# Performance work log

Hardware: AMD Instinct MI355X
Metric: run time of the kernel (lower is better)

## Reference

```python
import jax, jax.numpy as jnp
import numpy as np

B, TQ, TKV, D, H = 4, 1024, 2048, 1024, 16
DH = D // H


def setup_inputs() -> dict:
    key = jax.random.key(0)
    ks = jax.random.split(key, 12)
    s = 0.02
    return {
        "x": jax.random.normal(ks[0], (B, TQ, D), jnp.float32),
        "k_cache": jax.random.normal(ks[1], (B, TKV, D), jnp.float32),
        "v_cache": jax.random.normal(ks[2], (B, TKV, D), jnp.float32),
        "mask": jnp.zeros((TQ, TKV), jnp.float32),  # additive attention bias
        "Wq": jax.random.normal(ks[3], (D, D), jnp.float32) * s,
        "bq": jax.random.normal(ks[4], (D,), jnp.float32) * s,
        "Wk": jax.random.normal(ks[5], (D, D), jnp.float32) * s,  # key: no bias (Whisper-style)
        "Wv": jax.random.normal(ks[6], (D, D), jnp.float32) * s,
        "bv": jax.random.normal(ks[7], (D,), jnp.float32) * s,
        "Wo": jax.random.normal(ks[8], (D, D), jnp.float32) * s,
        "bo": jax.random.normal(ks[9], (D,), jnp.float32) * s,
    }


def reference(x, k_cache, v_cache, mask, Wq, bq, Wk, Wv, bv, Wo, bo):
    b, tq, d = x.shape
    scale = (d // H) ** -0.25
    # QKV projections (torch Linear: y = x @ W.T + b)
    q = x @ Wq.T + bq                      # [B,Tq,D]
    k_new = x @ Wk.T                       # [B,Tq,D] (key has no bias)
    v_new = x @ Wv.T + bv                  # [B,Tq,D]
    # KV-cache append: write last Tq positions
    k_cache = k_cache.at[:, -tq:, :].set(k_new)
    v_cache = v_cache.at[:, -tq:, :].set(v_new)
    # split heads
    qh = q.reshape(b, tq, H, DH) * scale           # [B,Tq,H,Dh]
    kh = k_cache.reshape(b, -1, H, DH) * scale     # [B,Tkv,H,Dh]
    vh = v_cache.reshape(b, -1, H, DH)             # [B,Tkv,H,Dh]
    qk = jnp.einsum("bqhd,bkhd->bhqk", qh, kh) + mask  # [B,H,Tq,Tkv]
    w = jax.nn.softmax(qk.astype(jnp.float32), axis=-1).astype(qh.dtype)
    wv = jnp.einsum("bhqk,bkhd->bqhd", w, vh).reshape(b, tq, d)
    out = wv @ Wo.T + bo
    return out, k_cache, v_cache
```

## Files before the change

kernel.cpp:

```cpp
#include <hip/hip_runtime.h>
#include <hip/hip_bf16.h>


typedef __bf16 bf16_t;
typedef __attribute__((ext_vector_type(4))) float f32x4;
typedef __attribute__((ext_vector_type(8))) __bf16 bf16x8;
typedef __attribute__((ext_vector_type(4))) __bf16 bf16x4;
typedef __attribute__((ext_vector_type(4))) unsigned short u16x4;

__device__ inline bf16x4 cvt4(float4 f) {
    bf16x4 o;
    o.x = (bf16_t)f.x; o.y = (bf16_t)f.y; o.z = (bf16_t)f.z; o.w = (bf16_t)f.w;
    return o;
}

__device__ inline void gload_lds16(const void* g, void* s) {
    __builtin_amdgcn_global_load_lds(
        (const __attribute__((address_space(1))) void*)g,
        (__attribute__((address_space(3))) void*)s, 16, 0, 0);
}

__device__ inline unsigned cvt_pk_bf16(float lo, float hi) {
    unsigned r;
    asm("v_cvt_pk_bf16_f32 %0, %1, %2" : "=v"(r) : "v"(lo), "v"(hi));
    return r;
}
__device__ inline void pswap32(unsigned& a, unsigned& b) {
    asm("v_permlane32_swap_b32 %0, %1" : "+v"(a), "+v"(b));
}
__device__ inline void pswap16(unsigned& a, unsigned& b) {
    asm("v_permlane16_swap_b32 %0, %1" : "+v"(a), "+v"(b));
}

#if __has_builtin(__builtin_amdgcn_exp2f)
__device__ inline float exp2_fast(float x) { return __builtin_amdgcn_exp2f(x); }
#else
__device__ inline float exp2_fast(float x) { return exp2f(x); }
#endif


__global__ void cast_f32_bf16_k(const float* __restrict__ src, bf16_t* __restrict__ dst, int n4) {
    int i = blockIdx.x * blockDim.x + threadIdx.x;
    if (i >= n4) return;
    float4 f = reinterpret_cast<const float4*>(src)[i];
    reinterpret_cast<bf16x4*>(dst)[i] = cvt4(f);
}

__global__ void build_wqkv_k(const float* __restrict__ Wq, const float* __restrict__ Wk,
                             const float* __restrict__ Wv, bf16_t* __restrict__ dst) {
    int i = blockIdx.x * blockDim.x + threadIdx.x;
    if (i >= 786432) return;
    int e0 = i * 4;
    int row = e0 >> 10;
    const float* src;
    if (row < 1024)       src = Wq + e0;
    else if (row < 2048)  src = Wk + (e0 - 1048576);
    else                  src = Wv + (e0 - 2097152);
    float4 f = *reinterpret_cast<const float4*>(src);
    reinterpret_cast<bf16x4*>(dst)[i] = cvt4(f);
}

__global__ void build_bias_k(const float* __restrict__ bq, const float* __restrict__ bv,
                             float* __restrict__ bias) {
    int i = blockIdx.x * blockDim.x + threadIdx.x;
    if (i >= 3072) return;
    float v;
    if (i < 1024)      v = bq[i];
    else if (i < 2048) v = 0.f;
    else               v = bv[i - 2048];
    bias[i] = v;
}

__global__ void copy_old2_k(const float* __restrict__ kc, const float* __restrict__ vc,
                            float* __restrict__ kout, float* __restrict__ vout,
                            bf16_t* __restrict__ k_bf) {
    int i = blockIdx.x * blockDim.x + threadIdx.x;
    if (i >= 2097152) return;
    int which = i >> 20;
    int ii = i & 1048575;
    int b = ii >> 18;
    int r = ii & 262143;
    size_t off = (size_t)b * 2097152 + (size_t)r * 4;
    if (which == 0) {
        float4 f = *reinterpret_cast<const float4*>(kc + off);
        *reinterpret_cast<float4*>(kout + off) = f;
        reinterpret_cast<bf16x4*>(k_bf + off)[0] = cvt4(f);
    } else {
        float4 f = *reinterpret_cast<const float4*>(vc + off);
        *reinterpret_cast<float4*>(vout + off) = f;
    }
}

__global__ __launch_bounds__(256) void transpose_v_k(const float* __restrict__ vout,
                                                     bf16_t* __restrict__ vT) {
    __shared__ bf16_t t[64][65];
    int blk = blockIdx.x;
    int kvt = blk >> 6;
    int bh  = blk & 63;
    int b = bh >> 4, h = bh & 15;
    int kv0 = kvt * 64;
    int tid = threadIdx.x;
    int c = tid & 63, r0 = tid >> 6;
    #pragma unroll
    for (int rr = r0; rr < 64; rr += 4)
        t[rr][c] = (bf16_t)vout[((size_t)b * 2048 + kv0 + rr) * 1024 + h * 64 + c];
    __syncthreads();
    #pragma unroll
    for (int dd = r0; dd < 64; dd += 4)
        vT[((size_t)bh * 64 + dd) * 2048 + kv0 + c] = t[c][dd];
}

__global__ void mask_bf16_k(const float* __restrict__ mask, bf16_t* __restrict__ maskB) {
    int i = blockIdx.x * blockDim.x + threadIdx.x;
    if (i >= 2097152) return;
    int r   = i & 3;
    int c16 = (i >> 2) & 15;
    int qd  = (i >> 6) & 3;
    int kb  = (i >> 8) & 127;
    int qb  = i >> 15;
    float v = mask[(size_t)(qb * 16 + c16) * 2048 + kb * 16 + qd * 4 + r] * 1.4426950408889634f;
    maskB[i] = (bf16_t)v;
}

template <int MODE>
__global__ __launch_bounds__(256) void gemm_lds_k(const bf16_t* __restrict__ A,
                                                  const bf16_t* __restrict__ Bw,
                                                  const float* __restrict__ bias,
                                                  bf16_t* __restrict__ q_bf,
                                                  float* __restrict__ kout,
                                                  bf16_t* __restrict__ k_bf,
                                                  float* __restrict__ vout,
                                                  float* __restrict__ out0) {
    const int K = 1024;
    __shared__ __align__(16) bf16_t As[2][4096];
    __shared__ __align__(16) bf16_t Bs[2][4096];
    int m0 = blockIdx.x * 128, n0 = blockIdx.y * 128;
    int tid = threadIdx.x;
    int lane = tid & 63, w = tid >> 6;
    int wr = w >> 1, wc = w & 1;
    int col16 = lane & 15, quad = lane >> 4;
    int mbase = m0 + wr * 64, nbase = n0 + wc * 64;

    int srow = tid >> 2;
    int scol = (tid & 3) * 8;
    const bf16_t* ga = A + (size_t)(m0 + srow) * K + scol;
    const bf16_t* gb = Bw + (size_t)(n0 + srow) * K + scol;

    f32x4 zero = {0.f, 0.f, 0.f, 0.f};
    f32x4 acc[4][4];
    #pragma unroll
    for (int mi = 0; mi < 4; mi++)
        #pragma unroll
        for (int ni = 0; ni < 4; ni++) acc[mi][ni] = zero;

    auto stageg = [&](int d, int k) {
        gload_lds16(ga + k, &As[d][tid * 8]);
        gload_lds16(ga + (size_t)64 * K + k, &As[d][tid * 8 + 2048]);
        gload_lds16(gb + k, &Bs[d][tid * 8]);
        gload_lds16(gb + (size_t)64 * K + k, &Bs[d][tid * 8 + 2048]);
    };

    stageg(0, 0);
    __syncthreads();
    for (int kb = 0; kb < 32; kb++) {
        int cur = kb & 1;
        if (kb < 31) stageg(cur ^ 1, (kb + 1) * 32);
        bf16x8 af[4], bfr[4];
        #pragma unroll
        for (int mi = 0; mi < 4; mi++)
            af[mi] = *reinterpret_cast<const bf16x8*>(
                &As[cur][(wr * 64 + mi * 16 + col16) * 32 + quad * 8]);
        #pragma unroll
        for (int ni = 0; ni < 4; ni++)
            bfr[ni] = *reinterpret_cast<const bf16x8*>(
                &Bs[cur][(wc * 64 + ni * 16 + col16) * 32 + quad * 8]);
        #pragma unroll
        for (int mi = 0; mi < 4; mi++)
            #pragma unroll
            for (int ni = 0; ni < 4; ni++)
                acc[mi][ni] = __builtin_amdgcn_mfma_f32_16x16x32_bf16(
                    af[mi], bfr[ni], acc[mi][ni], 0, 0, 0);
        __syncthreads();
    }

    #pragma unroll
    for (int mi = 0; mi < 4; mi++) {
        #pragma unroll
        for (int ni = 0; ni < 4; ni++) {
            int gm_base = mbase + mi * 16 + quad * 4;
            int gn = nbase + ni * 16 + col16;
            float bia = bias[gn];
            #pragma unroll
            for (int r = 0; r < 4; r++) {
                int gm = gm_base + r;
                float v = acc[mi][ni][r] + bia;
                if (MODE == 0) {
                    if (gn < 1024) {
                        q_bf[(size_t)gm * 1024 + gn] = (bf16_t)v;
                    } else if (gn < 2048) {
                        int n2 = gn - 1024;
                        int b = gm >> 10, t = gm & 1023;
                        size_t off = ((size_t)b * 2048 + 1024 + t) * 1024 + n2;
                        kout[off] = v;
                        k_bf[off] = (bf16_t)v;
                    } else {
                        int n2 = gn - 2048;
                        int b = gm >> 10, t = gm & 1023;
                        vout[((size_t)b * 2048 + 1024 + t) * 1024 + n2] = v;
                    }
                } else {
                    out0[(size_t)gm * 1024 + gn] = v;
                }
            }
        }
    }
}

__global__ __launch_bounds__(512, 4) void attn_k(const bf16_t* __restrict__ qbf,
                                                 const bf16_t* __restrict__ kbf,
                                                 const bf16_t* __restrict__ vT,
                                                 const bf16_t* __restrict__ maskB,
                                                 bf16_t* __restrict__ wv) {
    __shared__ __align__(16) bf16_t Ks[2][4096];
    __shared__ __align__(16) bf16_t Vs[2][4096];
    int logical = (blockIdx.x & 7) * 64 + (blockIdx.x >> 3);
    int bh = logical >> 3;
    int qtb = logical & 7;
    int b = bh >> 4, h = bh & 15;
    int tid = threadIdx.x, w = tid >> 6, lane = tid & 63;
    int col16 = lane & 15, quad = lane >> 4;
    int c7 = col16 & 7;
    int cx = (quad ^ c7) * 8;
    int qr0 = qtb * 128 + w * 16;

    int sr = tid >> 3, sc = (tid & 7) ^ ((tid >> 3) & 7);
    const bf16_t* kg = kbf + ((size_t)b * 2048 + sr) * 1024 + h * 64 + sc * 8;
    const bf16_t* vg = vT + ((size_t)bh * 64 + sr) * 2048 + sc * 8;
    auto stage = [&](int d, int kv0) {
        gload_lds16(kg + (size_t)kv0 * 1024, &Ks[d][tid * 8]);
        gload_lds16(vg + kv0, &Vs[d][tid * 8]);
    };

    const bf16_t* qrow = qbf + ((size_t)b * 1024 + qr0 + col16) * 1024 + h * 64;
    bf16x8 aq0 = *reinterpret_cast<const bf16x8*>(qrow + quad * 8);
    bf16x8 aq1 = *reinterpret_cast<const bf16x8*>(qrow + 32 + quad * 8);

    const bf16_t* mbase = maskB + (size_t)(qtb * 8 + w) * 32768 + quad * 64 + col16 * 4;

    f32x4 zero = {0.f, 0.f, 0.f, 0.f};
    f32x4 oacc[4];
    #pragma unroll
    for (int dt = 0; dt < 4; dt++) oacc[dt] = zero;
    float lrow = 0.f;

    stage(0, 0);
    __syncthreads();

    for (int t = 0; t < 32; t++) {
        int cur = t & 1;
        if (t < 31) stage(cur ^ 1, (t + 1) * 64);
        unsigned pk[4][2];
        #pragma unroll
        for (int nt = 0; nt < 4; nt++) {
            const bf16_t* kr = &Ks[cur][(nt * 16 + col16) * 64];
            bf16x8 k0 = *reinterpret_cast<const bf16x8*>(kr + cx);
            bf16x8 k1 = *reinterpret_cast<const bf16x8*>(kr + (cx ^ 32));
            f32x4 s = __builtin_amdgcn_mfma_f32_16x16x32_bf16(k0, aq0, zero, 0, 0, 0);
            s = __builtin_amdgcn_mfma_f32_16x16x32_bf16(k1, aq1, s, 0, 0, 0);
            u16x4 m4 = *reinterpret_cast<const u16x4*>(mbase + (size_t)(t * 4 + nt) * 256);
            float p[4];
            #pragma unroll
            for (int r = 0; r < 4; r++) {
                float mv = __builtin_bit_cast(float, (unsigned)m4[r] << 16);
                p[r] = exp2_fast(fmaf(s[r], 0.18033688011112042f, mv));
                lrow += p[r];
            }
            pk[nt][0] = cvt_pk_bf16(p[0], p[1]);
            pk[nt][1] = cvt_pk_bf16(p[2], p[3]);
        }
        union PB { unsigned u[4]; bf16x8 v; };
        PB pf0, pf1;
        {
            unsigned a0 = pk[0][0], b0 = pk[1][0];
            pswap32(a0, b0); pswap16(a0, b0);
            pf0.u[0] = a0; pf0.u[2] = b0;
            unsigned a1 = pk[0][1], b1 = pk[1][1];
            pswap32(a1, b1); pswap16(a1, b1);
            pf0.u[1] = a1; pf0.u[3] = b1;
            unsigned a2 = pk[2][0], b2 = pk[3][0];
            pswap32(a2, b2); pswap16(a2, b2);
            pf1.u[0] = a2; pf1.u[2] = b2;
            unsigned a3 = pk[2][1], b3 = pk[3][1];
            pswap32(a3, b3); pswap16(a3, b3);
            pf1.u[1] = a3; pf1.u[3] = b3;
        }
        #pragma unroll
        for (int dt = 0; dt < 4; dt++) {
            const bf16_t* vr = &Vs[cur][(dt * 16 + col16) * 64];
            bf16x8 v0 = *reinterpret_cast<const bf16x8*>(vr + cx);
            bf16x8 v1 = *reinterpret_cast<const bf16x8*>(vr + (cx ^ 32));
            oacc[dt] = __builtin_amdgcn_mfma_f32_16x16x32_bf16(v0, pf0.v, oacc[dt], 0, 0, 0);
            oacc[dt] = __builtin_amdgcn_mfma_f32_16x16x32_bf16(v1, pf1.v, oacc[dt], 0, 0, 0);
        }
        __syncthreads();
    }

    lrow += __shfl_xor(lrow, 16);
    lrow += __shfl_xor(lrow, 32);
    float inv = 1.f / lrow;
    bf16_t* orow = wv + ((size_t)b * 1024 + qr0 + col16) * 1024 + h * 64 + quad * 4;
    #pragma unroll
    for (int dt = 0; dt < 4; dt++) {
        bf16x4 o4;
        #pragma unroll
        for (int r = 0; r < 4; r++) o4[r] = (bf16_t)(oacc[dt][r] * inv);
        *reinterpret_cast<bf16x4*>(orow + dt * 16) = o4;
    }
}


extern "C" void kernel_launch(void* const* d_in, const int* in_sizes, int n_in,
                              void* d_out, int out_size, void* d_ws, size_t ws_size,
                              hipStream_t stream) {
    const float* x    = (const float*)d_in[0];
    const float* kc   = (const float*)d_in[1];
    const float* vc   = (const float*)d_in[2];
    const float* mask = (const float*)d_in[3];
    const float* Wq   = (const float*)d_in[4];
    const float* bq   = (const float*)d_in[5];
    const float* Wk   = (const float*)d_in[6];
    const float* Wv   = (const float*)d_in[7];
    const float* bv   = (const float*)d_in[8];
    const float* Wo   = (const float*)d_in[9];
    const float* bo   = (const float*)d_in[10];

    float* out0 = (float*)d_out;
    float* kout = out0 + 4194304;
    float* vout = out0 + 12582912;

    char* ws = (char*)d_ws;
    bf16_t* x_bf     = (bf16_t*)(ws);
    bf16_t* wqkv_bf  = (bf16_t*)(ws + 8388608);
    bf16_t* wo_bf    = (bf16_t*)(ws + 14680064);
    float*  bias_qkv = (float*)(ws + 16777216);
    bf16_t* q_bf     = (bf16_t*)(ws + 16789504);
    bf16_t* k_bf     = (bf16_t*)(ws + 25178112);
    bf16_t* vT_bf    = (bf16_t*)(ws + 41955328);
    bf16_t* wv_bf    = (bf16_t*)(ws + 58732544);
    bf16_t* maskB    = (bf16_t*)(ws + 67108864);

    cast_f32_bf16_k<<<4096, 256, 0, stream>>>(x, x_bf, 1048576);
    build_wqkv_k<<<3072, 256, 0, stream>>>(Wq, Wk, Wv, wqkv_bf);
    cast_f32_bf16_k<<<1024, 256, 0, stream>>>(Wo, wo_bf, 262144);
    build_bias_k<<<12, 256, 0, stream>>>(bq, bv, bias_qkv);
    mask_bf16_k<<<8192, 256, 0, stream>>>(mask, maskB);
    copy_old2_k<<<8192, 256, 0, stream>>>(kc, vc, kout, vout, k_bf);
    gemm_lds_k<0><<<dim3(32, 24), 256, 0, stream>>>(x_bf, wqkv_bf, bias_qkv,
                                                    q_bf, kout, k_bf, vout, nullptr);
    transpose_v_k<<<2048, 256, 0, stream>>>(vout, vT_bf);
    attn_k<<<512, 512, 0, stream>>>(q_bf, k_bf, vT_bf, maskB, wv_bf);
    gemm_lds_k<1><<<dim3(32, 8), 256, 0, stream>>>(wv_bf, wo_bf, bo,
                                                   nullptr, nullptr, nullptr, nullptr, out0);
}
```

Before: 313.5 us.

## Use 256x256-tile 8-wave pipelined GEMM for QKV projection; swizzle LDS in Wo GEMM

Replaces the QKV projection GEMM with a 256x256-tile, 512-thread kernel using BK=64. It uses XOR-swizzled LDS layouts, staggered A/B prefetch with explicit vmcnt waits, and barrier-separated MFMA phases with s_setprio. The Wo GEMM keeps its 128x128 tiling but gains an XOR swizzle on LDS reads and writes to reduce bank conflicts, and both epilogues are reordered so bias is loaded once per column. The aim is more data reuse per tile and better overlap of loads with MFMA. The cost is only 192 blocks for the QKV GEMM, which lowers occupancy, plus 128 KB of LDS per block.

Result: no change. 316.2 us (+0.9%).

```diff
diff --git a/kernel.cpp b/kernel.cpp
--- a/kernel.cpp
+++ b/kernel.cpp
@@ -122,15 +122,201 @@
     maskB[i] = (bf16_t)v;
 }
 
-template <int MODE>
-__global__ __launch_bounds__(256) void gemm_lds_k(const bf16_t* __restrict__ A,
+#define LDF(bufp, row, off) (*reinterpret_cast<const bf16x8*>(&(bufp)[(row) * 64 + (off)]))
+
+__global__ __launch_bounds__(512, 2) void gemm8_k(const bf16_t* __restrict__ A,
                                                   const bf16_t* __restrict__ Bw,
                                                   const float* __restrict__ bias,
                                                   bf16_t* __restrict__ q_bf,
                                                   float* __restrict__ kout,
                                                   bf16_t* __restrict__ k_bf,
-                                                  float* __restrict__ vout,
-                                                  float* __restrict__ out0) {
+                                                  float* __restrict__ vout) {
+    const int K = 1024;
+    __shared__ __align__(16) bf16_t As[2][16384];
+    __shared__ __align__(16) bf16_t Bs[2][16384];
+    int m0 = blockIdx.x * 256, n0 = blockIdx.y * 256;
+    int tid = threadIdx.x;
+    int lane = tid & 63, w = tid >> 6;
+    int wrM = w >> 2, wrN = w & 3;
+    int col16 = lane & 15, quad = lane >> 4;
+    int cx = (quad ^ (col16 & 7)) * 8;
+
+    int sr = tid >> 3;
+    int scb = ((tid & 7) ^ (sr & 7)) * 8;
+    const bf16_t* ga = A + (size_t)(m0 + sr) * K + scb;
+    const bf16_t* gb = Bw + (size_t)(n0 + sr) * K + scb;
+    int ldst = sr * 64 + (tid & 7) * 8;
+
+    auto stageA = [&](int d, int kt) {
+        size_t ko = (size_t)kt * 64;
+        gload_lds16(ga + ko, &As[d][ldst]);
+        gload_lds16(ga + 64 * (size_t)K + ko, &As[d][ldst + 4096]);
+        gload_lds16(ga + 128 * (size_t)K + ko, &As[d][ldst + 8192]);
+        gload_lds16(ga + 192 * (size_t)K + ko, &As[d][ldst + 12288]);
+    };
+    auto stageB = [&](int d, int kt) {
+        size_t ko = (size_t)kt * 64;
+        gload_lds16(gb + ko, &Bs[d][ldst]);
+        gload_lds16(gb + 64 * (size_t)K + ko, &Bs[d][ldst + 4096]);
+        gload_lds16(gb + 128 * (size_t)K + ko, &Bs[d][ldst + 8192]);
+        gload_lds16(gb + 192 * (size_t)K + ko, &Bs[d][ldst + 12288]);
+    };
+
+    int arow = wrM * 128 + col16;
+    int brow = wrN * 64 + col16;
+
+    f32x4 zero = {0.f, 0.f, 0.f, 0.f};
+    f32x4 acc[8][4];
+    #pragma unroll
+    for (int mi = 0; mi < 8; mi++)
+        #pragma unroll
+        for (int ni = 0; ni < 4; ni++) acc[mi][ni] = zero;
+
+    stageA(0, 0);
+    stageB(0, 0);
+    stageA(1, 1);
+    asm volatile("s_waitcnt vmcnt(4)" ::: "memory");
+    __builtin_amdgcn_s_barrier();
+
+    for (int kt = 0; kt < 16; kt++) {
+        int d = kt & 1;
+        const bf16_t* Ad = As[d];
+        const bf16_t* Bd = Bs[d];
+        bf16x8 a0[4][2], bb0[2][2];
+        #pragma unroll
+        for (int mi = 0; mi < 4; mi++) {
+            a0[mi][0] = LDF(Ad, arow + mi * 16, cx);
+            a0[mi][1] = LDF(Ad, arow + mi * 16, cx ^ 32);
+        }
+        #pragma unroll
+        for (int ni = 0; ni < 2; ni++) {
+            bb0[ni][0] = LDF(Bd, brow + ni * 16, cx);
+            bb0[ni][1] = LDF(Bd, brow + ni * 16, cx ^ 32);
+        }
+        if (kt < 15) stageB(d ^ 1, kt + 1);
+        __builtin_amdgcn_s_barrier();
+        __builtin_amdgcn_s_setprio(1);
+        #pragma unroll
+        for (int mi = 0; mi < 4; mi++)
+            #pragma unroll
+            for (int ni = 0; ni < 2; ni++) {
+                acc[mi][ni] = __builtin_amdgcn_mfma_f32_16x16x32_bf16(a0[mi][0], bb0[ni][0], acc[mi][ni], 0, 0, 0);
+                acc[mi][ni] = __builtin_amdgcn_mfma_f32_16x16x32_bf16(a0[mi][1], bb0[ni][1], acc[mi][ni], 0, 0, 0);
+            }
+        __builtin_amdgcn_s_setprio(0);
+        __builtin_amdgcn_s_barrier();
+        bf16x8 bb1[2][2];
+        #pragma unroll
+        for (int ni = 0; ni < 2; ni++) {
+            bb1[ni][0] = LDF(Bd, brow + 32 + ni * 16, cx);
+            bb1[ni][1] = LDF(Bd, brow + 32 + ni * 16, cx ^ 32);
+        }
+        __builtin_amdgcn_s_barrier();
+        __builtin_amdgcn_s_setprio(1);
+        #pragma unroll
+        for (int mi = 0; mi < 4; mi++)
+            #pragma unroll
+            for (int ni = 0; ni < 2; ni++) {
+                acc[mi][ni + 2] = __builtin_amdgcn_mfma_f32_16x16x32_bf16(a0[mi][0], bb1[ni][0], acc[mi][ni + 2], 0, 0, 0);
+                acc[mi][ni + 2] = __builtin_amdgcn_mfma_f32_16x16x32_bf16(a0[mi][1], bb1[ni][1], acc[mi][ni + 2], 0, 0, 0);
+            }
+        __builtin_amdgcn_s_setprio(0);
+        __builtin_amdgcn_s_barrier();
+        bf16x8 a1[4][2];
+        #pragma unroll
+        for (int mi = 0; mi < 4; mi++) {
+            a1[mi][0] = LDF(Ad, arow + 64 + mi * 16, cx);
+            a1[mi][1] = LDF(Ad, arow + 64 + mi * 16, cx ^ 32);
+        }
+        __builtin_amdgcn_s_barrier();
+        __builtin_amdgcn_s_setprio(1);
+        #pragma unroll
+        for (int mi = 0; mi < 4; mi++)
+            #pragma unroll
+            for (int ni = 0; ni < 2; ni++) {
+                acc[mi + 4][ni] = __builtin_amdgcn_mfma_f32_16x16x32_bf16(a1[mi][0], bb0[ni][0], acc[mi + 4][ni], 0, 0, 0);
+                acc[mi + 4][ni] = __builtin_amdgcn_mfma_f32_16x16x32_bf16(a1[mi][1], bb0[ni][1], acc[mi + 4][ni], 0, 0, 0);
+            }
+        __builtin_amdgcn_s_setprio(0);
+        __builtin_amdgcn_s_barrier();
+        if (kt < 14) {
+            stageA(d, kt + 2);
+            asm volatile("s_waitcnt vmcnt(4)" ::: "memory");
+        } else {
+            asm volatile("s_waitcnt vmcnt(0)" ::: "memory");
+        }
+        __builtin_amdgcn_s_barrier();
+        __builtin_amdgcn_s_setprio(1);
+        #pragma unroll
+        for (int mi = 0; mi < 4; mi++)
+            #pragma unroll
+            for (int ni = 0; ni < 2; ni++) {
+                acc[mi + 4][ni + 2] = __builtin_amdgcn_mfma_f32_16x16x32_bf16(a1[mi][0], bb1[ni][0], acc[mi + 4][ni + 2], 0, 0, 0);
+                acc[mi + 4][ni + 2] = __builtin_amdgcn_mfma_f32_16x16x32_bf16(a1[mi][1], bb1[ni][1], acc[mi + 4][ni + 2], 0, 0, 0);
+            }
+        __builtin_amdgcn_s_setprio(0);
+        __builtin_amdgcn_s_barrier();
+    }
+
+    int mb = m0 + wrM * 128 + quad * 4;
+    int nb = n0 + wrN * 64 + col16;
+    if (n0 < 1024) {
+        #pragma unroll
+        for (int ni = 0; ni < 4; ni++) {
+            int gn = nb + ni * 16;
+            float bia = bias[gn];
+            #pragma unroll
+            for (int mi = 0; mi < 8; mi++) {
+                int gm = mb + mi * 16;
+                #pragma unroll
+                for (int r = 0; r < 4; r++)
+                    q_bf[(size_t)(gm + r) * 1024 + gn] = (bf16_t)(acc[mi][ni][r] + bia);
+            }
+        }
+    } else if (n0 < 2048) {
+        #pragma unroll
+        for (int ni = 0; ni < 4; ni++) {
+            int gn = nb + ni * 16;
+            float bia = bias[gn];
+            int n2 = gn - 1024;
+            #pragma unroll
+            for (int mi = 0; mi < 8; mi++) {
+                int gm = mb + mi * 16;
+                #pragma unroll
+                for (int r = 0; r < 4; r++) {
+                    int gmr = gm + r;
+                    int b = gmr >> 10, t = gmr & 1023;
+                    size_t off = ((size_t)b * 2048 + 1024 + t) * 1024 + n2;
+                    float v = acc[mi][ni][r] + bia;
+                    kout[off] = v;
+                    k_bf[off] = (bf16_t)v;
+                }
+            }
+        }
+    } else {
+        #pragma unroll
+        for (int ni = 0; ni < 4; ni++) {
+            int gn = nb + ni * 16;
+            float bia = bias[gn];
+            int n2 = gn - 2048;
+            #pragma unroll
+            for (int mi = 0; mi < 8; mi++) {
+                int gm = mb + mi * 16;
+                #pragma unroll
+                for (int r = 0; r < 4; r++) {
+                    int gmr = gm + r;
+                    int b = gmr >> 10, t = gmr & 1023;
+                    vout[((size_t)b * 2048 + 1024 + t) * 1024 + n2] = acc[mi][ni][r] + bia;
+                }
+            }
+        }
+    }
+}
+
+__global__ __launch_bounds__(256) void gemm_wo_k(const bf16_t* __restrict__ A,
+                                                 const bf16_t* __restrict__ Bw,
+                                                 const float* __restrict__ bias,
+                                                 float* __restrict__ out0) {
     const int K = 1024;
     __shared__ __align__(16) bf16_t As[2][4096];
     __shared__ __align__(16) bf16_t Bs[2][4096];
@@ -139,12 +325,13 @@
     int lane = tid & 63, w = tid >> 6;
     int wr = w >> 1, wc = w & 1;
     int col16 = lane & 15, quad = lane >> 4;
-    int mbase = m0 + wr * 64, nbase = n0 + wc * 64;
 
     int srow = tid >> 2;
-    int scol = (tid & 3) * 8;
+    int scol = ((tid & 3) ^ ((srow >> 1) & 3)) * 8;
     const bf16_t* ga = A + (size_t)(m0 + srow) * K + scol;
     const bf16_t* gb = Bw + (size_t)(n0 + srow) * K + scol;
+
+    int qsw = (quad ^ ((col16 >> 1) & 3)) * 8;
 
     f32x4 zero = {0.f, 0.f, 0.f, 0.f};
     f32x4 acc[4][4];
@@ -169,11 +356,11 @@
         #pragma unroll
         for (int mi = 0; mi < 4; mi++)
             af[mi] = *reinterpret_cast<const bf16x8*>(
-                &As[cur][(wr * 64 + mi * 16 + col16) * 32 + quad * 8]);
+                &As[cur][(wr * 64 + mi * 16 + col16) * 32 + qsw]);
         #pragma unroll
         for (int ni = 0; ni < 4; ni++)
             bfr[ni] = *reinterpret_cast<const bf16x8*>(
-                &Bs[cur][(wc * 64 + ni * 16 + col16) * 32 + quad * 8]);
+                &Bs[cur][(wc * 64 + ni * 16 + col16) * 32 + qsw]);
         #pragma unroll
         for (int mi = 0; mi < 4; mi++)
             #pragma unroll
@@ -183,35 +370,18 @@
         __syncthreads();
     }
 
-    #pragma unroll
-    for (int mi = 0; mi < 4; mi++) {
-        #pragma unroll
-        for (int ni = 0; ni < 4; ni++) {
-            int gm_base = mbase + mi * 16 + quad * 4;
-            int gn = nbase + ni * 16 + col16;
-            float bia = bias[gn];
-            #pragma unroll
-            for (int r = 0; r < 4; r++) {
-                int gm = gm_base + r;
-                float v = acc[mi][ni][r] + bia;
-                if (MODE == 0) {
-                    if (gn < 1024) {
-                        q_bf[(size_t)gm * 1024 + gn] = (bf16_t)v;
-                    } else if (gn < 2048) {
-                        int n2 = gn - 1024;
-                        int b = gm >> 10, t = gm & 1023;
-                        size_t off = ((size_t)b * 2048 + 1024 + t) * 1024 + n2;
-                        kout[off] = v;
-                        k_bf[off] = (bf16_t)v;
-                    } else {
-                        int n2 = gn - 2048;
-                        int b = gm >> 10, t = gm & 1023;
-                        vout[((size_t)b * 2048 + 1024 + t) * 1024 + n2] = v;
-                    }
-                } else {
-                    out0[(size_t)gm * 1024 + gn] = v;
-                }
-            }
+    int mbase = m0 + wr * 64 + quad * 4;
+    int nbase = n0 + wc * 64 + col16;
+    #pragma unroll
+    for (int ni = 0; ni < 4; ni++) {
+        int gn = nbase + ni * 16;
+        float bia = bias[gn];
+        #pragma unroll
+        for (int mi = 0; mi < 4; mi++) {
+            int gm = mbase + mi * 16;
+            #pragma unroll
+            for (int r = 0; r < 4; r++)
+                out0[(size_t)(gm + r) * 1024 + gn] = acc[mi][ni][r] + bia;
         }
     }
 }
@@ -355,10 +525,9 @@
     build_bias_k<<<12, 256, 0, stream>>>(bq, bv, bias_qkv);
     mask_bf16_k<<<8192, 256, 0, stream>>>(mask, maskB);
     copy_old2_k<<<8192, 256, 0, stream>>>(kc, vc, kout, vout, k_bf);
-    gemm_lds_k<0><<<dim3(32, 24), 256, 0, stream>>>(x_bf, wqkv_bf, bias_qkv,
-                                                    q_bf, kout, k_bf, vout, nullptr);
+    gemm8_k<<<dim3(16, 12), 512, 0, stream>>>(x_bf, wqkv_bf, bias_qkv,
+                                              q_bf, kout, k_bf, vout);
     transpose_v_k<<<2048, 256, 0, stream>>>(vout, vT_bf);
     attn_k<<<512, 512, 0, stream>>>(q_bf, k_bf, vT_bf, maskB, wv_bf);
-    gemm_lds_k<1><<<dim3(32, 8), 256, 0, stream>>>(wv_bf, wo_bf, bo,
-                                                   nullptr, nullptr, nullptr, nullptr, out0);
-}
+    gemm_wo_k<<<dim3(32, 8), 256, 0, stream>>>(wv_bf, wo_bf, bo, out0);
+}
```
